# Kernel optimization log

Hardware: AMD Instinct MI355X
Metric: run time of the kernel (lower is better)

## Reference

```python
import jax, jax.numpy as jnp
import numpy as np

B, T, E, H = 8, 2048, 1024, 64

def setup_inputs() -> dict:
    key = jax.random.key(0)
    kx, kk, kq, kv = jax.random.split(key, 4)
    x = jax.random.normal(kx, (B, T, E), dtype=jnp.float32)
    # nn.Linear weight init scale ~ 1/sqrt(fan_in); use small normal weights
    s = 1.0 / np.sqrt(E)
    Wk = jax.random.normal(kk, (E, H), dtype=jnp.float32) * s
    Wq = jax.random.normal(kq, (E, H), dtype=jnp.float32) * s
    Wv = jax.random.normal(kv, (E, H), dtype=jnp.float32) * s
    return {"x": x, "Wk": Wk, "Wq": Wq, "Wv": Wv}

def reference(x, Wk, Wq, Wv):
    # x: [B,T,E]; projections to head_size H
    k = jnp.einsum('bte,eh->bth', x, Wk)
    q = jnp.einsum('bte,eh->bth', x, Wq)
    v = jnp.einsum('bte,eh->bth', x, Wv)
    # NOTE: original scales by num_embds**-0.5 (E, not head_size)
    scale = jnp.asarray(E, x.dtype) ** -0.5
    wei = jnp.einsum('bqh,bkh->bqk', q, k) * scale  # [B,T,T]
    causal = jnp.tril(jnp.ones((T, T), dtype=bool))
    wei = jnp.where(causal, wei, -jnp.inf)
    wei = jax.nn.softmax(wei, axis=-1)
    # dropout p=0.0 -> identity (eval-mode deterministic baseline)
    out = jnp.einsum('bqk,bkh->bqh', wei, v)  # [B,T,H]
    return out
```

## Files before the change

### kernel.cpp

```cpp
#include <hip/hip_runtime.h>
#include <hip/hip_bf16.h>

#define B_ 8
#define T_ 2048
#define E_ 1024
#define H_ 64

typedef __attribute__((ext_vector_type(8))) short short8v;
typedef __attribute__((ext_vector_type(4))) float f32x4;

__device__ __forceinline__ unsigned short bfbits(float f) {
  return __builtin_bit_cast(unsigned short, __float2bfloat16(f));
}

__device__ __forceinline__ void gload_lds16(const void* g, void* l) {
  __builtin_amdgcn_global_load_lds(
      (const __attribute__((address_space(1))) unsigned*)g,
      (__attribute__((address_space(3))) unsigned*)l, 16, 0, 0);
}

__global__ __launch_bounds__(256) void prep_wf(
    const float* __restrict__ Wk, const float* __restrict__ Wq,
    const float* __restrict__ Wv, __hip_bfloat16* __restrict__ Wf) {
  const int idx = blockIdx.x * 256 + threadIdx.x;
  const int f = idx >> 9;
  const int e = idx & 511;
  const int l = e >> 3, j = e & 7;
  const int cf = f >> 5, kb = f & 31;
  const int m = cf >> 2;
  const int c = (cf & 3) * 16 + (l & 15);
  const int k = kb * 32 + (l >> 4) * 8 + j;
  const float* W = (m == 0) ? Wk : (m == 1) ? Wq : Wv;
  float v = W[k * H_ + c];
  if (m == 1) v *= 0.03125f;
  Wf[idx] = __float2bfloat16(v);
}

__global__ __launch_bounds__(512) void proj_mfma(
    const float* __restrict__ x, const __hip_bfloat16* __restrict__ Wf,
    __hip_bfloat16* __restrict__ Qb, __hip_bfloat16* __restrict__ Kb,
    __hip_bfloat16* __restrict__ Vt) {
  __shared__ float xs[4][32][64];
  __shared__ __hip_bfloat16 rep[8][16][24];
  const int tid = threadIdx.x;
  const int lane = tid & 63;
  const int w = tid >> 6;
  const int rowg = w >> 2;
  const int colh = w & 3;
  const int cf0 = colh * 3;
  const int r = lane & 15, g = lane >> 4;
  const int r0 = blockIdx.x * 32;
  const int rw0 = r0 + rowg * 16;

  f32x4 acc[3];
  #pragma unroll
  for (int i = 0; i < 3; ++i) acc[i] = (f32x4){0.f, 0.f, 0.f, 0.f};

  auto stage = [&](int buf, int kc) {
    const int row = w * 4 + (lane >> 4);
    const int sl = lane & 15;
    const int ssl = (sl & 8) | ((sl & 7) ^ (row & 7));
    gload_lds16(x + (size_t)(r0 + row) * E_ + kc + ssl * 4, &xs[buf][w * 4][0]);
  };

  auto loadW = [&](int t, short8v (&Wn)[3][2]) {
    #pragma unroll
    for (int i = 0; i < 3; ++i)
      #pragma unroll
      for (int h = 0; h < 2; ++h)
        Wn[i][h] = *(const short8v*)(
            Wf + (((size_t)(cf0 + i) * 32 + t * 2 + h) << 9) + lane * 8);
  };

  auto computeStep = [&](int buf, short8v (&Wc)[3][2]) {
    const char* base = (const char*)&xs[buf][0][0] + (rowg * 16 + r) * 256;
    #pragma unroll
    for (int h = 0; h < 2; ++h) {
      const int s0 = h * 8 + ((2 * g + 0) ^ (r & 7));
      const int s1 = h * 8 + ((2 * g + 1) ^ (r & 7));
      const f32x4 lo = *(const f32x4*)(base + s0 * 16);
      const f32x4 hi = *(const f32x4*)(base + s1 * 16);
      short8v A;
      A[0] = (short)bfbits(lo[0]); A[1] = (short)bfbits(lo[1]);
      A[2] = (short)bfbits(lo[2]); A[3] = (short)bfbits(lo[3]);
      A[4] = (short)bfbits(hi[0]); A[5] = (short)bfbits(hi[1]);
      A[6] = (short)bfbits(hi[2]); A[7] = (short)bfbits(hi[3]);
      #pragma unroll
      for (int i = 0; i < 3; ++i)
        acc[i] = __builtin_amdgcn_mfma_f32_16x16x32_bf16(A, Wc[i][h], acc[i], 0, 0, 0);
    }
  };

  short8v WA[3][2], WB[3][2];
  loadW(0, WA);
  stage(0, 0);
  stage(1, 64);
  stage(2, 128);
  asm volatile("s_waitcnt vmcnt(2)" ::: "memory");
  __builtin_amdgcn_s_barrier();

  for (int t = 0; t < 16; t += 2) {
    if (t + 3 < 16) stage((t + 3) & 3, (t + 3) * 64);
    loadW(t + 1, WB);
    computeStep(t & 3, WA);
    if (t < 14) asm volatile("s_waitcnt vmcnt(8)" ::: "memory");
    else        asm volatile("s_waitcnt vmcnt(6)" ::: "memory");
    __builtin_amdgcn_s_barrier();
    if (t + 4 < 16) stage((t + 4) & 3, (t + 4) * 64);
    if (t + 2 < 16) loadW(t + 2, WA);
    computeStep((t + 1) & 3, WB);
    if (t < 12) {
      asm volatile("s_waitcnt vmcnt(8)" ::: "memory");
      __builtin_amdgcn_s_barrier();
    } else if (t == 12) {
      asm volatile("s_waitcnt vmcnt(7)" ::: "memory");
      __builtin_amdgcn_s_barrier();
    }
  }

  __hip_bfloat16* rp = &rep[w][0][0];
  #pragma unroll
  for (int i = 0; i < 3; ++i) {
    const int cf = cf0 + i;
    const int m = cf >> 2;
    const int c0 = (cf & 3) * 16;
    if (m < 2) {
      __hip_bfloat16* Pout = (m == 0) ? Kb : Qb;
      #pragma unroll
      for (int reg = 0; reg < 4; ++reg)
        rp[(g * 4 + reg) * 24 + r] = __float2bfloat16(acc[i][reg]);
      asm volatile("s_waitcnt lgkmcnt(0)" ::: "memory");
      __builtin_amdgcn_sched_barrier(0);
      if (lane < 32) {
        const int row = lane >> 1, ch = lane & 1;
        *(uint4*)(Pout + (size_t)(rw0 + row) * H_ + c0 + ch * 8) =
            *(const uint4*)(rp + row * 24 + ch * 8);
      }
      asm volatile("s_waitcnt lgkmcnt(0)" ::: "memory");
      __builtin_amdgcn_sched_barrier(0);
    } else {
      const int b = r0 >> 11;
      const int tt = (rw0 & 2047) + g * 4;
      ushort4 pk;
      pk.x = bfbits(acc[i][0]); pk.y = bfbits(acc[i][1]);
      pk.z = bfbits(acc[i][2]); pk.w = bfbits(acc[i][3]);
      *(ushort4*)(Vt + (size_t)(b * 64 + c0 + r) * T_ + tt) = pk;
    }
  }
}

__global__ __launch_bounds__(128, 2) void attn_mfma(
    const __hip_bfloat16* __restrict__ Qb, const __hip_bfloat16* __restrict__ Kb,
    const __hip_bfloat16* __restrict__ Vt, float* __restrict__ out) {
  __shared__ __hip_bfloat16 Ps[2][16][72];
  __shared__ float cmb[64][20];
  __shared__ float ml[16][2];
  const int tid = threadIdx.x;
  const int lane = tid & 63;
  const int w = tid >> 6;
  const int r = lane & 15, g = lane >> 4;
  const int blk = blockIdx.x;
  const int b = blk & 7;
  const int i = blk >> 3;
  const int s_ = i >> 5, j_ = i & 31;
  const int qt = (s_ == 0) ? j_ : (s_ == 1) ? (63 - j_) : (s_ == 2) ? (64 + j_) : (127 - j_);
  const int q0 = qt * 16;
  const size_t tb = (size_t)b * T_;
  const int bb = b * 64;

  const short8v qf0 = *(const short8v*)(Qb + (tb + q0 + r) * H_ + g * 8);
  const short8v qf1 = *(const short8v*)(Qb + (tb + q0 + r) * H_ + 32 + g * 8);

  f32x4 o[4];
  #pragma unroll
  for (int k2 = 0; k2 < 4; ++k2) o[k2] = (f32x4){0.f, 0.f, 0.f, 0.f};
  float mrun = -1e30f, lrun = 0.f;

  const int nt = (qt >> 2) + 1;
  const int h_ = (nt + 1) >> 1;
  const int t0 = w ? h_ : 0;
  const int t1 = w ? nt : h_;

  short8v kbA[4][2], kbB[4][2];
  auto loadK = [&](int t, short8v (&kb)[4][2]) {
    #pragma unroll
    for (int kg = 0; kg < 4; ++kg)
      #pragma unroll
      for (int c = 0; c < 2; ++c)
        kb[kg][c] = *(const short8v*)(Kb + (tb + t * 64 + kg * 16 + r) * H_ + c * 32 + g * 8);
  };

  auto body = [&](int t, short8v (&kbU)[4][2], short8v (&kbP)[4][2]) {
    short8v vb[4][2];
    #pragma unroll
    for (int hg = 0; hg < 4; ++hg)
      #pragma unroll
      for (int c = 0; c < 2; ++c)
        vb[hg][c] = *(const short8v*)(
            Vt + (size_t)(bb + hg * 16 + r) * T_ + t * 64 + c * 32 + g * 8);
    if (t + 1 < t1) loadK(t + 1, kbP);

    f32x4 s[4];
    #pragma unroll
    for (int k2 = 0; k2 < 4; ++k2) s[k2] = (f32x4){0.f, 0.f, 0.f, 0.f};
    __builtin_amdgcn_s_setprio(1);
    #pragma unroll
    for (int kg = 0; kg < 4; ++kg) {
      s[kg] = __builtin_amdgcn_mfma_f32_16x16x32_bf16(kbU[kg][0], qf0, s[kg], 0, 0, 0);
      s[kg] = __builtin_amdgcn_mfma_f32_16x16x32_bf16(kbU[kg][1], qf1, s[kg], 0, 0, 0);
    }
    __builtin_amdgcn_s_setprio(0);

    if (t == nt - 1) {
      #pragma unroll
      for (int kg = 0; kg < 4; ++kg)
        #pragma unroll
        for (int reg = 0; reg < 4; ++reg)
          if (t * 64 + kg * 16 + g * 4 + reg > q0 + r) s[kg][reg] = -1e30f;
    }

    float pm = s[0][0];
    #pragma unroll
    for (int kg = 0; kg < 4; ++kg)
      #pragma unroll
      for (int reg = 0; reg < 4; ++reg) pm = fmaxf(pm, s[kg][reg]);
    pm = fmaxf(pm, __shfl_xor(pm, 16));
    pm = fmaxf(pm, __shfl_xor(pm, 32));
    const float nm = fmaxf(mrun, pm);
    const float al = __expf(mrun - nm);
    mrun = nm;
    float p[4][4];
    float rs = 0.f;
    #pragma unroll
    for (int kg = 0; kg < 4; ++kg)
      #pragma unroll
      for (int reg = 0; reg < 4; ++reg) {
        p[kg][reg] = __expf(s[kg][reg] - nm);
        rs += p[kg][reg];
      }
    rs += __shfl_xor(rs, 16);
    rs += __shfl_xor(rs, 32);
    lrun = lrun * al + rs;
    #pragma unroll
    for (int hg = 0; hg < 4; ++hg) o[hg] *= al;

    #pragma unroll
    for (int kg = 0; kg < 4; ++kg) {
      ushort4 u;
      u.x = bfbits(p[kg][0]); u.y = bfbits(p[kg][1]);
      u.z = bfbits(p[kg][2]); u.w = bfbits(p[kg][3]);
      *(ushort4*)&Ps[w][r][kg * 16 + g * 4] = u;
    }
    short8v pf[2];
    pf[0] = *(const short8v*)&Ps[w][r][g * 8];
    pf[1] = *(const short8v*)&Ps[w][r][32 + g * 8];

    __builtin_amdgcn_s_setprio(1);
    #pragma unroll
    for (int c = 0; c < 2; ++c)
      #pragma unroll
      for (int hg = 0; hg < 4; ++hg)
        o[hg] = __builtin_amdgcn_mfma_f32_16x16x32_bf16(vb[hg][c], pf[c], o[hg], 0, 0, 0);
    __builtin_amdgcn_s_setprio(0);
  };

  if (t0 < t1) {
    loadK(t0, kbA);
    int t = t0;
    while (true) {
      body(t, kbA, kbB);
      if (++t >= t1) break;
      body(t, kbB, kbA);
      if (++t >= t1) break;
    }
  }

  if (w == 1) {
    if (g == 0) { ml[r][0] = mrun; ml[r][1] = lrun; }
    #pragma unroll
    for (int hg = 0; hg < 4; ++hg) *(f32x4*)&cmb[lane][hg * 4] = o[hg];
  }
  __syncthreads();
  if (w == 0) {
    const float m1 = ml[r][0], l1 = ml[r][1];
    const float mm = fmaxf(mrun, m1);
    const float sc0 = __expf(mrun - mm), sc1 = __expf(m1 - mm);
    const float inv = 1.f / (lrun * sc0 + l1 * sc1);
    #pragma unroll
    for (int hg = 0; hg < 4; ++hg) {
      const f32x4 o1 = *(const f32x4*)&cmb[lane][hg * 4];
      f32x4 res = (o[hg] * sc0 + o1 * sc1) * inv;
      *(f32x4*)(out + (tb + q0 + r) * H_ + hg * 16 + g * 4) = res;
    }
  }
}

extern "C" void kernel_launch(void* const* d_in, const int* in_sizes, int n_in,
                              void* d_out, int out_size, void* d_ws, size_t ws_size,
                              hipStream_t stream) {
  const float* x  = (const float*)d_in[0];
  const float* Wk = (const float*)d_in[1];
  const float* Wq = (const float*)d_in[2];
  const float* Wv = (const float*)d_in[3];
  float* out = (float*)d_out;

  __hip_bfloat16* Qb = (__hip_bfloat16*)d_ws;
  __hip_bfloat16* Kb = Qb + (size_t)B_ * T_ * H_;
  __hip_bfloat16* Vt = Kb + (size_t)B_ * T_ * H_;
  __hip_bfloat16* Wf = Vt + (size_t)B_ * T_ * H_;

  prep_wf<<<(12 * 32 * 512) / 256, 256, 0, stream>>>(Wk, Wq, Wv, Wf);
  proj_mfma<<<(B_ * T_) / 32, 512, 0, stream>>>(x, Wf, Qb, Kb, Vt);
  attn_mfma<<<B_ * (T_ / 16), 128, 0, stream>>>(Qb, Kb, Vt, out);
}
```

Baseline: 64.02 us.

## Preload whole x tile as bf16 in LDS instead of streaming fp32 chunks

The projection kernel now loads the block's entire 32x1024 x tile up front, converts it to bf16 once and stores it swizzled in LDS. The multi-stage global_load_lds pipeline with explicit waitcnt/barrier handshakes is removed, leaving only W-fragment double buffering in the main loop. Column-fragment assignment is also remapped (m*4+colh) so each wave's outputs go to K, Q and V uniformly. This cuts per-step conversion work and barriers, but LDS use rises to 64KB and the x loads are no longer overlapped with MFMA compute.

```diff
diff --git a/kernel.cpp b/kernel.cpp
--- a/kernel.cpp
+++ b/kernel.cpp
@@ -11,12 +11,6 @@
 
 __device__ __forceinline__ unsigned short bfbits(float f) {
   return __builtin_bit_cast(unsigned short, __float2bfloat16(f));
-}
-
-__device__ __forceinline__ void gload_lds16(const void* g, void* l) {
-  __builtin_amdgcn_global_load_lds(
-      (const __attribute__((address_space(1))) unsigned*)g,
-      (__attribute__((address_space(3))) unsigned*)l, 16, 0, 0);
 }
 
 __global__ __launch_bounds__(256) void prep_wf(
@@ -40,113 +34,97 @@
     const float* __restrict__ x, const __hip_bfloat16* __restrict__ Wf,
     __hip_bfloat16* __restrict__ Qb, __hip_bfloat16* __restrict__ Kb,
     __hip_bfloat16* __restrict__ Vt) {
-  __shared__ float xs[4][32][64];
+  __shared__ __hip_bfloat16 xp[32 * 128 * 8];
   __shared__ __hip_bfloat16 rep[8][16][24];
   const int tid = threadIdx.x;
   const int lane = tid & 63;
   const int w = tid >> 6;
   const int rowg = w >> 2;
   const int colh = w & 3;
-  const int cf0 = colh * 3;
   const int r = lane & 15, g = lane >> 4;
   const int r0 = blockIdx.x * 32;
-  const int rw0 = r0 + rowg * 16;
+
+  {
+    const int row = tid >> 4;
+    const int ci = tid & 15;
+    const float* src = x + (size_t)(r0 + row) * E_ + ci * 8;
+    char* dst = (char*)xp + row * 2048;
+    #pragma unroll
+    for (int j = 0; j < 8; ++j) {
+      const f32x4 lo = *(const f32x4*)(src + j * 128);
+      const f32x4 hi = *(const f32x4*)(src + j * 128 + 4);
+      short8v t8;
+      t8[0] = (short)bfbits(lo[0]); t8[1] = (short)bfbits(lo[1]);
+      t8[2] = (short)bfbits(lo[2]); t8[3] = (short)bfbits(lo[3]);
+      t8[4] = (short)bfbits(hi[0]); t8[5] = (short)bfbits(hi[1]);
+      t8[6] = (short)bfbits(hi[2]); t8[7] = (short)bfbits(hi[3]);
+      const int sl = ci + 16 * j;
+      const int ss = (sl & 120) | ((sl & 7) ^ (row & 7));
+      *(short8v*)(dst + ss * 16) = t8;
+    }
+  }
+  __syncthreads();
 
   f32x4 acc[3];
   #pragma unroll
-  for (int i = 0; i < 3; ++i) acc[i] = (f32x4){0.f, 0.f, 0.f, 0.f};
-
-  auto stage = [&](int buf, int kc) {
-    const int row = w * 4 + (lane >> 4);
-    const int sl = lane & 15;
-    const int ssl = (sl & 8) | ((sl & 7) ^ (row & 7));
-    gload_lds16(x + (size_t)(r0 + row) * E_ + kc + ssl * 4, &xs[buf][w * 4][0]);
-  };
-
-  auto loadW = [&](int t, short8v (&Wn)[3][2]) {
-    #pragma unroll
-    for (int i = 0; i < 3; ++i)
+  for (int m = 0; m < 3; ++m) acc[m] = (f32x4){0.f, 0.f, 0.f, 0.f};
+
+  const int arow = rowg * 16 + r;
+  const char* abase = (const char*)xp + arow * 2048;
+
+  short8v WA[6], WB[6];
+  auto loadW = [&](int t, short8v (&Wn)[6]) {
+    #pragma unroll
+    for (int m = 0; m < 3; ++m)
       #pragma unroll
       for (int h = 0; h < 2; ++h)
-        Wn[i][h] = *(const short8v*)(
-            Wf + (((size_t)(cf0 + i) * 32 + t * 2 + h) << 9) + lane * 8);
-  };
-
-  auto computeStep = [&](int buf, short8v (&Wc)[3][2]) {
-    const char* base = (const char*)&xs[buf][0][0] + (rowg * 16 + r) * 256;
-    #pragma unroll
-    for (int h = 0; h < 2; ++h) {
-      const int s0 = h * 8 + ((2 * g + 0) ^ (r & 7));
-      const int s1 = h * 8 + ((2 * g + 1) ^ (r & 7));
-      const f32x4 lo = *(const f32x4*)(base + s0 * 16);
-      const f32x4 hi = *(const f32x4*)(base + s1 * 16);
-      short8v A;
-      A[0] = (short)bfbits(lo[0]); A[1] = (short)bfbits(lo[1]);
-      A[2] = (short)bfbits(lo[2]); A[3] = (short)bfbits(lo[3]);
-      A[4] = (short)bfbits(hi[0]); A[5] = (short)bfbits(hi[1]);
-      A[6] = (short)bfbits(hi[2]); A[7] = (short)bfbits(hi[3]);
-      #pragma unroll
-      for (int i = 0; i < 3; ++i)
-        acc[i] = __builtin_amdgcn_mfma_f32_16x16x32_bf16(A, Wc[i][h], acc[i], 0, 0, 0);
-    }
-  };
-
-  short8v WA[3][2], WB[3][2];
+        Wn[m * 2 + h] = *(const short8v*)(
+            Wf + (((size_t)(m * 4 + colh) * 32 + t * 2 + h) << 9) + lane * 8);
+  };
+  auto computeT = [&](int t, short8v (&Wc)[6]) {
+    #pragma unroll
+    for (int kh = 0; kh < 2; ++kh) {
+      const int slot = t * 8 + kh * 4 + g;
+      const int ss = (slot & 120) | ((slot & 7) ^ (arow & 7));
+      const short8v A = *(const short8v*)(abase + ss * 16);
+      #pragma unroll
+      for (int m = 0; m < 3; ++m)
+        acc[m] = __builtin_amdgcn_mfma_f32_16x16x32_bf16(A, Wc[m * 2 + kh], acc[m], 0, 0, 0);
+    }
+  };
+
   loadW(0, WA);
-  stage(0, 0);
-  stage(1, 64);
-  stage(2, 128);
-  asm volatile("s_waitcnt vmcnt(2)" ::: "memory");
-  __builtin_amdgcn_s_barrier();
-
+  #pragma unroll
   for (int t = 0; t < 16; t += 2) {
-    if (t + 3 < 16) stage((t + 3) & 3, (t + 3) * 64);
-    loadW(t + 1, WB);
-    computeStep(t & 3, WA);
-    if (t < 14) asm volatile("s_waitcnt vmcnt(8)" ::: "memory");
-    else        asm volatile("s_waitcnt vmcnt(6)" ::: "memory");
-    __builtin_amdgcn_s_barrier();
-    if (t + 4 < 16) stage((t + 4) & 3, (t + 4) * 64);
+    if (t + 1 < 16) loadW(t + 1, WB);
+    computeT(t, WA);
     if (t + 2 < 16) loadW(t + 2, WA);
-    computeStep((t + 1) & 3, WB);
-    if (t < 12) {
-      asm volatile("s_waitcnt vmcnt(8)" ::: "memory");
-      __builtin_amdgcn_s_barrier();
-    } else if (t == 12) {
-      asm volatile("s_waitcnt vmcnt(7)" ::: "memory");
-      __builtin_amdgcn_s_barrier();
-    }
+    computeT(t + 1, WB);
   }
 
   __hip_bfloat16* rp = &rep[w][0][0];
   #pragma unroll
-  for (int i = 0; i < 3; ++i) {
-    const int cf = cf0 + i;
-    const int m = cf >> 2;
-    const int c0 = (cf & 3) * 16;
-    if (m < 2) {
-      __hip_bfloat16* Pout = (m == 0) ? Kb : Qb;
-      #pragma unroll
-      for (int reg = 0; reg < 4; ++reg)
-        rp[(g * 4 + reg) * 24 + r] = __float2bfloat16(acc[i][reg]);
-      asm volatile("s_waitcnt lgkmcnt(0)" ::: "memory");
-      __builtin_amdgcn_sched_barrier(0);
-      if (lane < 32) {
-        const int row = lane >> 1, ch = lane & 1;
-        *(uint4*)(Pout + (size_t)(rw0 + row) * H_ + c0 + ch * 8) =
-            *(const uint4*)(rp + row * 24 + ch * 8);
-      }
-      asm volatile("s_waitcnt lgkmcnt(0)" ::: "memory");
-      __builtin_amdgcn_sched_barrier(0);
-    } else {
-      const int b = r0 >> 11;
-      const int tt = (rw0 & 2047) + g * 4;
-      ushort4 pk;
-      pk.x = bfbits(acc[i][0]); pk.y = bfbits(acc[i][1]);
-      pk.z = bfbits(acc[i][2]); pk.w = bfbits(acc[i][3]);
-      *(ushort4*)(Vt + (size_t)(b * 64 + c0 + r) * T_ + tt) = pk;
-    }
-  }
+  for (int m = 0; m < 2; ++m) {
+    __hip_bfloat16* Pout = (m == 0) ? Kb : Qb;
+    #pragma unroll
+    for (int reg = 0; reg < 4; ++reg)
+      rp[(g * 4 + reg) * 24 + r] = __float2bfloat16(acc[m][reg]);
+    asm volatile("s_waitcnt lgkmcnt(0)" ::: "memory");
+    __builtin_amdgcn_sched_barrier(0);
+    if (lane < 32) {
+      const int row = lane >> 1, ch = lane & 1;
+      *(uint4*)(Pout + (size_t)(r0 + rowg * 16 + row) * H_ + colh * 16 + ch * 8) =
+          *(const uint4*)(rp + row * 24 + ch * 8);
+    }
+    asm volatile("s_waitcnt lgkmcnt(0)" ::: "memory");
+    __builtin_amdgcn_sched_barrier(0);
+  }
+  const int b = r0 >> 11;
+  const int tt = (r0 & 2047) + rowg * 16 + g * 4;
+  ushort4 pk;
+  pk.x = bfbits(acc[2][0]); pk.y = bfbits(acc[2][1]);
+  pk.z = bfbits(acc[2][2]); pk.w = bfbits(acc[2][3]);
+  *(ushort4*)(Vt + (size_t)(b * 64 + colh * 16 + r) * T_ + tt) = pk;
 }
 
 __global__ __launch_bounds__(128, 2) void attn_mfma(
```

Result: slower. 67.37 us (+5.2%).
